# Kernel tuning notes

Hardware: AMD Instinct MI355X
Metric: run time of the kernel (lower is better)

## Reference

```python
import jax, jax.numpy as jnp
import numpy as np

B, N, D, K, H = 4, 128, 256, 128, 32
A, E = 128, 512  # num_atoms, num_edges (edge types)


def _nonlinear(x, W1, b1, W2, b2):
    # torch NonLinear: Linear -> exact GELU -> Linear
    return jax.nn.gelu(x @ W1 + b1, approximate=False) @ W2 + b2


def setup_inputs() -> dict:
    key = jax.random.key(0)
    ks = jax.random.split(key, 32)
    pos = jax.random.normal(ks[0], (B, N, 3), dtype=jnp.float32) * 3.0
    x = jax.random.randint(ks[1], (B, N, 9), 1, A + 1)          # avoid padding idx 0
    node_type_edge = jax.random.randint(ks[2], (B, N, N, 2), 1, E)
    # 9 atom embedding tables, padding_idx=0 rows zeroed
    atom_emb = (jax.random.normal(ks[3], (9, A + 1, D), dtype=jnp.float32) * 0.02).at[:, 0].set(0.0)
    sc = D ** -0.5
    W_la = jax.random.normal(ks[4], (D, D), dtype=jnp.float32) * sc
    W_ra = jax.random.normal(ks[5], (D, D), dtype=jnp.float32) * sc
    W_ld = jax.random.normal(ks[6], (D, D), dtype=jnp.float32) * sc
    W_rd = jax.random.normal(ks[7], (D, D), dtype=jnp.float32) * sc
    gbf_means = jax.random.normal(ks[8], (K,), dtype=jnp.float32)
    gbf_stds = jax.random.uniform(ks[9], (K,), dtype=jnp.float32, minval=0.5, maxval=3.0)
    src_mul = (jax.random.normal(ks[10], (E,), dtype=jnp.float32) * 0.1).at[0].set(0.0)
    tgt_mul = (jax.random.normal(ks[11], (E,), dtype=jnp.float32) * 0.1).at[0].set(0.0)
    src_bias = (jax.random.normal(ks[12], (E,), dtype=jnp.float32) * 0.1).at[0].set(0.0)
    tgt_bias = (jax.random.normal(ks[13], (E,), dtype=jnp.float32) * 0.1).at[0].set(0.0)
    gbf_W1 = jax.random.normal(ks[14], (K, K), dtype=jnp.float32) * (K ** -0.5)
    gbf_b1 = jnp.zeros((K,), jnp.float32)
    gbf_W2 = jax.random.normal(ks[15], (K, H), dtype=jnp.float32) * (K ** -0.5)
    gbf_b2 = jnp.zeros((H,), jnp.float32)
    dih_W1 = jax.random.normal(ks[16], (D, D), dtype=jnp.float32) * sc
    dih_b1 = jnp.zeros((D,), jnp.float32)
    dih_W2 = jax.random.normal(ks[17], (D, H), dtype=jnp.float32) * sc
    dih_b2 = jnp.zeros((H,), jnp.float32)
    ang_W1 = jax.random.normal(ks[18], (D, D), dtype=jnp.float32) * sc
    ang_b1 = jnp.zeros((D,), jnp.float32)
    ang_W2 = jax.random.normal(ks[19], (D, D), dtype=jnp.float32) * sc
    ang_b2 = jnp.zeros((D,), jnp.float32)
    return dict(pos=pos, atom_emb=atom_emb, W_la=W_la, W_ra=W_ra, W_ld=W_ld, W_rd=W_rd,
                gbf_means=gbf_means, gbf_stds=gbf_stds, src_mul=src_mul, tgt_mul=tgt_mul,
                src_bias=src_bias, tgt_bias=tgt_bias, gbf_W1=gbf_W1, gbf_b1=gbf_b1,
                gbf_W2=gbf_W2, gbf_b2=gbf_b2, dih_W1=dih_W1, dih_b1=dih_b1, dih_W2=dih_W2,
                dih_b2=dih_b2, ang_W1=ang_W1, ang_b1=ang_b1, ang_W2=ang_W2, ang_b2=ang_b2,
                x=x, node_type_edge=node_type_edge)


def _forward(pos, atom_emb, W_la, W_ra, W_ld, W_rd, gbf_means, gbf_stds,
             src_mul, tgt_mul, src_bias, tgt_bias, gbf_W1, gbf_b1, gbf_W2, gbf_b2,
             dih_W1, dih_b1, dih_W2, dih_b2, ang_W1, ang_b1, ang_W2, ang_b2,
             x, node_type_edge):
    no_pos = (~jnp.all(pos == 0, axis=(-1, -2))).astype(pos.dtype)  # [B]
    # sum of 9 per-feature embeddings  -> [B, N, D]
    node_feature = sum(atom_emb[i][x[..., i]] for i in range(9))
    padding_mask = jnp.all(x == 0, axis=-1)                         # [B, N]
    # delta_pos[b,i,j] = pos[b,j] - pos[b,i]
    delta_pos = pos[:, None, :, :] - pos[:, :, None, :]             # [B, N, N, 3]
    dist = jnp.linalg.norm(delta_pos, axis=-1)                      # [B, N, N]
    delta_pos = delta_pos / (dist[..., None] + 1e-5)
    # node_vec_feature[b,i,c,d] = node_feature[b,i,d] * sum_j (1-pad_j) delta_pos[b,i,j,c]
    # (exact fusion of edge_vec_feature -> masked sum, since node_feature only depends on i)
    keep = (~padding_mask).astype(pos.dtype)                        # [B, N]
    s = jnp.einsum('bijc,bj->bic', delta_pos, keep)                 # [B, N, 3]
    node_vec = node_feature[:, :, None, :] * s[..., None]           # [B, N, 3, D]
    # angle feature
    angle = jnp.sum((node_vec @ W_la) * (node_vec @ W_ra), axis=-2)  # [B, N, D]
    angle = _nonlinear(angle, ang_W1, ang_b1, ang_W2, ang_b2)
    angle = angle * no_pos[:, None, None]
    # gaussian RPE
    et = node_type_edge
    mul = src_mul[et[..., 0]] + tgt_mul[et[..., 1]]                 # [B, N, N]
    bias = src_bias[et[..., 0]] + tgt_bias[et[..., 1]]
    xg = mul[..., None] * dist[..., None] + bias[..., None]         # [B, N, N, 1] -> K
    std = jnp.abs(gbf_stds) + 0.01
    a = (2.0 * 3.14159) ** 0.5
    edge_feature = jnp.exp(-0.5 * ((xg - gbf_means) / std) ** 2) / (a * std)  # [B,N,N,K]
    gbf_result = _nonlinear(edge_feature, gbf_W1, gbf_b1, gbf_W2, gbf_b2)     # [B,N,N,H]
    # dihedral: vector rejection of projected node vec features onto edge directions
    left = node_vec @ W_ld                                          # [B, N, 3, D]
    right = node_vec @ W_rd
    Ld = jnp.einsum('bjcd,bijc->bijd', left, delta_pos)             # proj of left (indexed j)
    wl = left[:, None] - Ld[..., None, :] * delta_pos[..., None]    # [B, N, N, 3, D]
    Rd = jnp.einsum('bicd,bijc->bijd', right, -delta_pos)           # proj of right (indexed i)
    wr = right[:, :, None] - Rd[..., None, :] * (-delta_pos)[..., None]
    edge_dih = jnp.sum(wl * wr, axis=-2)                            # [B, N, N, D]
    edge_dih = _nonlinear(edge_dih, dih_W1, dih_b1, dih_W2, dih_b2)  # [B, N, N, H]
    attn_bias = (gbf_result + edge_dih) * no_pos[:, None, None, None]
    attn_bias = jnp.transpose(attn_bias, (0, 3, 1, 2))              # [B, H, N, N]
    attn_bias = jnp.where(padding_mask[:, None, None, :], -jnp.inf, attn_bias)
    return attn_bias, angle, delta_pos


def reference(pos, atom_emb, W_la, W_ra, W_ld, W_rd, gbf_means, gbf_stds,
              src_mul, tgt_mul, src_bias, tgt_bias, gbf_W1, gbf_b1, gbf_W2, gbf_b2,
              dih_W1, dih_b1, dih_W2, dih_b2, ang_W1, ang_b1, ang_W2, ang_b2,
              x, node_type_edge):
    return _forward(pos, atom_emb, W_la, W_ra, W_ld, W_rd, gbf_means, gbf_stds,
                    src_mul, tgt_mul, src_bias, tgt_bias, gbf_W1, gbf_b1, gbf_W2, gbf_b2,
                    dih_W1, dih_b1, dih_W2, dih_b2, ang_W1, ang_b1, ang_W2, ang_b2,
                    x, node_type_edge)
```

## Files before the change

kernel.cpp:

```cpp
#include <hip/hip_runtime.h>
#include <math.h>

#define BB 4
#define NN 128
#define DD 256
#define KK 128
#define HH 32
#define AA 128
#define EE 512

typedef float f32x4 __attribute__((ext_vector_type(4)));
typedef short short8 __attribute__((ext_vector_type(8)));

__device__ __forceinline__ float gelu_fast(float x) {
    float x2 = x * x;
    float t = x * fmaf(x2, 0.0713548162726f, 1.59576912161f);
    float e = __expf(-t);
    return x * __builtin_amdgcn_rcpf(1.0f + e);
}

__device__ __forceinline__ unsigned short f2bf(float f) {
    unsigned int u = __float_as_uint(f);
    u = u + 0x7fffu + ((u >> 16) & 1u);
    return (unsigned short)(u >> 16);
}

__device__ __forceinline__ int swz512(int row, int colByte) {
    return row * 512 + (colByte ^ ((row & 7) << 4));
}
__device__ __forceinline__ int swz256(int row, int colByte) {
    return row * 256 + (colByte ^ ((row & 7) << 4));
}

__global__ __launch_bounds__(256) void k_setup(
    const float* __restrict__ pos, const int* __restrict__ x,
    const float* __restrict__ atom_emb,
    const float* __restrict__ dW1, const float* __restrict__ dW2,
    const float* __restrict__ gW1, const float* __restrict__ gW2,
    const float* __restrict__ wla, const float* __restrict__ wra,
    const float* __restrict__ wld, const float* __restrict__ wrd,
    const float* __restrict__ aW1, const float* __restrict__ aW2,
    float* __restrict__ out_dp, float* __restrict__ dist_ws,
    float* __restrict__ s_ws, float* __restrict__ keep, float* __restrict__ no_pos,
    unsigned short* __restrict__ nf_ws, unsigned short* __restrict__ wpack) {
    int blk = blockIdx.x;
    int t = threadIdx.x;

    if (blk < 512) {
        int bi = blk;
        int b = bi >> 7;
        int i = bi & 127;
        __shared__ float red[3][128];
        __shared__ int flag;
        if (t == 0) flag = 0;
        float kj = 0.0f, dx = 0.0f, dy = 0.0f, dz = 0.0f;
        float pjx = 0.0f, pjy = 0.0f, pjz = 0.0f;
        int bj = b * NN + (t & 127);
        if (t < 128) {
            int j = t;
            int allz = 1;
            #pragma unroll
            for (int f = 0; f < 9; ++f) allz &= (x[bj * 9 + f] == 0);
            kj = allz ? 0.0f : 1.0f;
            float pix = pos[bi * 3 + 0], piy = pos[bi * 3 + 1], piz = pos[bi * 3 + 2];
            pjx = pos[bj * 3 + 0]; pjy = pos[bj * 3 + 1]; pjz = pos[bj * 3 + 2];
            dx = pjx - pix; dy = pjy - piy; dz = pjz - piz;
            float dist = sqrtf(dx * dx + dy * dy + dz * dz);
            float inv = 1.0f / (dist + 1e-5f);
            dx *= inv; dy *= inv; dz *= inv;
            size_t e = (size_t)bi * NN + j;
            out_dp[e * 3 + 0] = dx;
            out_dp[e * 3 + 1] = dy;
            out_dp[e * 3 + 2] = dz;
            dist_ws[e] = dist;
            red[0][j] = kj * dx; red[1][j] = kj * dy; red[2][j] = kj * dz;
        }
        __syncthreads();
        if (t < 128) {
            if (pjx != 0.0f || pjy != 0.0f || pjz != 0.0f) flag = 1;
        }
        for (int off = 64; off > 0; off >>= 1) {
            if (t < off) {
                red[0][t] += red[0][t + off];
                red[1][t] += red[1][t + off];
                red[2][t] += red[2][t + off];
            }
            __syncthreads();
        }
        if (t == 0) {
            s_ws[bi * 3 + 0] = red[0][0];
            s_ws[bi * 3 + 1] = red[1][0];
            s_ws[bi * 3 + 2] = red[2][0];
        }
        if (i == 0 && t < 128) {
            keep[bj] = kj;
            if (t == 0) no_pos[b] = flag ? 1.0f : 0.0f;
        }
        return;
    }

    if (blk < 1024) {
        int bn = blk - 512;
        float acc = 0.0f;
        #pragma unroll
        for (int f = 0; f < 9; ++f) {
            int xi = x[bn * 9 + f];
            acc += atom_emb[((size_t)(f * (AA + 1) + xi)) * DD + t];
        }
        nf_ws[(size_t)bn * DD + t] = f2bf(acc);
        return;
    }

    {
        int idx = (blk - 1024) * 256 + t;
        const float* W; int Nc, base, k, c8;
        if (idx < 8192)       { W = dW1; Nc = 256; base = 0;     int li = idx;         k = li >> 5; c8 = li & 31; }
        else if (idx < 9216)  { W = dW2; Nc = 32;  base = 65536; int li = idx - 8192;  k = li >> 2; c8 = li & 3; }
        else if (idx < 11264) { W = gW1; Nc = 128; base = 73728; int li = idx - 9216;  k = li >> 4; c8 = li & 15; }
        else if (idx < 11776) { W = gW2; Nc = 32;  base = 90112; int li = idx - 11264; k = li >> 2; c8 = li & 3; }
        else if (idx < 60928) {
            int q  = (idx - 11776) >> 13;
            int li = (idx - 11776) & 8191;
            W = (q == 0) ? wla : (q == 1) ? wra : (q == 2) ? wld : (q == 3) ? wrd : (q == 4) ? aW1 : aW2;
            Nc = 256; base = 94208 + q * 65536; k = li >> 5; c8 = li & 31;
        }
        else return;
        int ntiles = Nc >> 4;
        int ks = k >> 5, hi = (k & 31) >> 3, ee = k & 7;
        const float* wp = &W[k * Nc + c8 * 8];
        float4 a = *reinterpret_cast<const float4*>(wp);
        float4 b4 = *reinterpret_cast<const float4*>(wp + 4);
        float vals[8] = {a.x, a.y, a.z, a.w, b4.x, b4.y, b4.z, b4.w};
        #pragma unroll
        for (int jj = 0; jj < 8; ++jj) {
            int c = c8 * 8 + jj;
            int nt = c >> 4, lo = c & 15;
            wpack[base + (((ks * ntiles + nt) * 64) + hi * 16 + lo) * 8 + ee] = f2bf(vals[jj]);
        }
    }
}

__device__ __forceinline__ void stage32x256(const unsigned short* __restrict__ src, int bn0,
                                            unsigned short* sA, int t) {
    #pragma unroll
    for (int r = 0; r < 4; ++r) {
        int idx = r * 256 + t;
        int row = idx >> 5;
        int c8 = idx & 31;
        short8 v = *reinterpret_cast<const short8*>(&src[((size_t)(bn0 + row)) * DD + c8 * 8]);
        *reinterpret_cast<short8*>((char*)sA + swz512(row, c8 * 16)) = v;
    }
}

__device__ __forceinline__ void gemm_nt(const unsigned short* __restrict__ Bp, int nt,
                                        const unsigned short* sA, int l, int lo, int hi,
                                        f32x4 acc[2]) {
    for (int ks = 0; ks < 8; ++ks) {
        short8 a0 = *reinterpret_cast<const short8*>((const char*)sA + swz512(lo, ks * 64 + hi * 16));
        short8 a1 = *reinterpret_cast<const short8*>((const char*)sA + swz512(16 + lo, ks * 64 + hi * 16));
        short8 bfr = *reinterpret_cast<const short8*>(&Bp[(((size_t)ks * 16 + nt) * 64 + l) * 8]);
        acc[0] = __builtin_amdgcn_mfma_f32_16x16x32_bf16(a0, bfr, acc[0], 0, 0, 0);
        acc[1] = __builtin_amdgcn_mfma_f32_16x16x32_bf16(a1, bfr, acc[1], 0, 0, 0);
    }
}

__device__ __forceinline__ void gemm_chunk32(const unsigned short* __restrict__ Bp,
                                             const unsigned short* sAp,
                                             int w, int l, int lo, int hi,
                                             f32x4 acc[2][4]) {
    for (int ks = 0; ks < 8; ++ks) {
        short8 a[2];
        #pragma unroll
        for (int m = 0; m < 2; ++m)
            a[m] = *reinterpret_cast<const short8*>((const char*)sAp + swz512(m * 16 + lo, ks * 64 + hi * 16));
        #pragma unroll
        for (int n = 0; n < 4; ++n) {
            short8 bfr = *reinterpret_cast<const short8*>(&Bp[(((size_t)ks * 16 + (w * 4 + n)) * 64 + l) * 8]);
            #pragma unroll
            for (int m = 0; m < 2; ++m)
                acc[m][n] = __builtin_amdgcn_mfma_f32_16x16x32_bf16(a[m], bfr, acc[m][n], 0, 0, 0);
        }
    }
}

__global__ __launch_bounds__(256, 4) void k2a(
    const unsigned short* __restrict__ nf_ws,
    const unsigned short* __restrict__ Wla_p, const unsigned short* __restrict__ Wra_p,
    const unsigned short* __restrict__ Wld_p, const unsigned short* __restrict__ Wrd_p,
    const float* __restrict__ s_ws,
    float* __restrict__ ld_ws, float* __restrict__ rd_ws,
    unsigned short* __restrict__ ap_ws) {
    int blk = blockIdx.x;
    int c = blk & 3, tile = blk >> 2;
    int bn0 = tile * 32;
    int t = threadIdx.x;
    int w = t >> 6, l = t & 63, lo = l & 15, hi = l >> 4;
    int nt = c * 4 + w;

    __shared__ __align__(16) unsigned short sA[32 * 256];
    __shared__ float ls2[32];
    if (t < 32) {
        float a0 = s_ws[(bn0 + t) * 3 + 0];
        float a1 = s_ws[(bn0 + t) * 3 + 1];
        float a2 = s_ws[(bn0 + t) * 3 + 2];
        ls2[t] = a0 * a0 + a1 * a1 + a2 * a2;
    }
    stage32x256(nf_ws, bn0, sA, t);
    __syncthreads();

    f32x4 a_la[2] = {}, a_ra[2] = {}, a_ld[2] = {}, a_rd[2] = {};
    gemm_nt(Wla_p, nt, sA, l, lo, hi, a_la);
    gemm_nt(Wra_p, nt, sA, l, lo, hi, a_ra);
    gemm_nt(Wld_p, nt, sA, l, lo, hi, a_ld);
    gemm_nt(Wrd_p, nt, sA, l, lo, hi, a_rd);

    int col = nt * 16 + lo;
    #pragma unroll
    for (int m = 0; m < 2; ++m) {
        #pragma unroll
        for (int r = 0; r < 4; ++r) {
            int row = m * 16 + hi * 4 + r;
            size_t off = (size_t)(bn0 + row) * DD + col;
            ld_ws[off] = a_ld[m][r];
            rd_ws[off] = a_rd[m][r];
            ap_ws[off] = f2bf(ls2[row] * a_la[m][r] * a_ra[m][r]);
        }
    }
}

__global__ __launch_bounds__(256, 2) void k_mega(
    const unsigned short* __restrict__ Wp1, const unsigned short* __restrict__ Wp2,
    const unsigned short* __restrict__ Wg1, const unsigned short* __restrict__ Wg2,
    const unsigned short* __restrict__ WaW1_p, const unsigned short* __restrict__ WaW2_p,
    const float* __restrict__ dih_b1, const float* __restrict__ dih_b2,
    const float* __restrict__ gbf_b1, const float* __restrict__ gbf_b2,
    const float* __restrict__ ang_b1, const float* __restrict__ ang_b2,
    const float* __restrict__ gbf_means, const float* __restrict__ gbf_stds,
    const float* __restrict__ src_mul, const float* __restrict__ tgt_mul,
    const float* __restrict__ src_bias, const float* __restrict__ tgt_bias,
    const int* __restrict__ nte,
    const unsigned short* __restrict__ ap_ws,
    const float* __restrict__ ld_ws, const float* __restrict__ rd_ws,
    const float* __restrict__ s_ws, const float* __restrict__ dist_ws,
    const float* __restrict__ keep, const float* __restrict__ no_pos,
    const float* __restrict__ dp_in,
    float* __restrict__ out_angle, float* __restrict__ out_attn) {
    int t = threadIdx.x;
    int w  = t >> 6;
    int l  = t & 63;
    int lo = l & 15;
    int hi = l >> 4;

    __shared__ __align__(16) unsigned short sE[64 * 256];
    __shared__ __align__(16) unsigned short sH[64 * 256];
    __shared__ __align__(16) float rd_l[DD];
    __shared__ float sg[64], sxg[64], skeep[64];
    __shared__ __align__(16) float lmean[KK], linv[KK], lcoef[KK];

    if (blockIdx.x < 16) {
        int tile = blockIdx.x;
        int bn0 = tile * 32;
        stage32x256(ap_ws, bn0, sE, t);
        __syncthreads();
        {
            f32x4 acc[2][4] = {};
            gemm_chunk32(WaW1_p, sE, w, l, lo, hi, acc);
            #pragma unroll
            for (int n = 0; n < 4; ++n) {
                int col = w * 64 + n * 16 + lo;
                float b1v = ang_b1[col];
                #pragma unroll
                for (int m = 0; m < 2; ++m)
                    #pragma unroll
                    for (int r = 0; r < 4; ++r) {
                        int row = m * 16 + hi * 4 + r;
                        *reinterpret_cast<unsigned short*>((char*)sH + swz512(row, col * 2)) =
                            f2bf(gelu_fast(acc[m][n][r] + b1v));
                    }
            }
        }
        __syncthreads();
        {
            f32x4 acc[2][4] = {};
            gemm_chunk32(WaW2_p, sH, w, l, lo, hi, acc);
            float lnp = no_pos[tile >> 2];
            #pragma unroll
            for (int n = 0; n < 4; ++n) {
                int col = w * 64 + n * 16 + lo;
                float b2v = ang_b2[col];
                #pragma unroll
                for (int m = 0; m < 2; ++m)
                    #pragma unroll
                    for (int r = 0; r < 4; ++r) {
                        int row = m * 16 + hi * 4 + r;
                        out_angle[(size_t)(bn0 + row) * DD + col] = (acc[m][n][r] + b2v) * lnp;
                    }
            }
        }
        return;
    }

    int blk = blockIdx.x - 16;
    int jh = blk & 1;
    int i  = (blk >> 1) & 127;
    int b  = blk >> 8;
    int j0 = jh * 64;

    int bi = b * NN + i;

    if (t < 64) {
        int j = j0 + t;
        size_t e = (size_t)bi * NN + j;
        float d0 = dp_in[e * 3 + 0], d1 = dp_in[e * 3 + 1], d2 = dp_in[e * 3 + 2];
        float si0 = s_ws[bi * 3 + 0], si1 = s_ws[bi * 3 + 1], si2 = s_ws[bi * 3 + 2];
        int bj = b * NN + j;
        float sj0 = s_ws[bj * 3 + 0], sj1 = s_ws[bj * 3 + 1], sj2 = s_ws[bj * 3 + 2];
        float u = sj0 * d0 + sj1 * d1 + sj2 * d2;
        float v = si0 * d0 + si1 * d1 + si2 * d2;
        float dp2 = d0 * d0 + d1 * d1 + d2 * d2;
        sg[t] = (si0 * sj0 + si1 * sj1 + si2 * sj2) - u * v * (2.0f - dp2);
        int et0 = nte[e * 2 + 0], et1 = nte[e * 2 + 1];
        sxg[t] = (src_mul[et0] + tgt_mul[et1]) * dist_ws[e] + src_bias[et0] + tgt_bias[et1];
        skeep[t] = keep[bj];
    } else if (t < 128) {
        int q = t - 64;
        reinterpret_cast<float4*>(rd_l)[q] =
            reinterpret_cast<const float4*>(&rd_ws[(size_t)bi * DD])[q];
    } else {
        int k = t - 128;
        float s = fabsf(gbf_stds[k]) + 0.01f;
        lmean[k] = gbf_means[k];
        linv[k] = 1.0f / s;
        lcoef[k] = 1.0f / (2.5066262f * s);
    }
    __syncthreads();

    {
        const float* ldbase = &ld_ws[((size_t)(b * NN + j0)) * DD];
        #pragma unroll
        for (int r = 0; r < 8; ++r) {
            int idx = r * 256 + t;
            int row = idx >> 5;
            int c8  = idx & 31;
            float g = sg[row];
            const float* lp = ldbase + row * DD + c8 * 8;
            float4 l0 = *reinterpret_cast<const float4*>(lp);
            float4 l1 = *reinterpret_cast<const float4*>(lp + 4);
            float4 r0 = *reinterpret_cast<const float4*>(&rd_l[c8 * 8]);
            float4 r1 = *reinterpret_cast<const float4*>(&rd_l[c8 * 8 + 4]);
            short8 vv;
            vv[0] = (short)f2bf(g * l0.x * r0.x);
            vv[1] = (short)f2bf(g * l0.y * r0.y);
            vv[2] = (short)f2bf(g * l0.z * r0.z);
            vv[3] = (short)f2bf(g * l0.w * r0.w);
            vv[4] = (short)f2bf(g * l1.x * r1.x);
            vv[5] = (short)f2bf(g * l1.y * r1.y);
            vv[6] = (short)f2bf(g * l1.z * r1.z);
            vv[7] = (short)f2bf(g * l1.w * r1.w);
            *reinterpret_cast<short8*>((char*)sE + swz512(row, c8 * 16)) = vv;
        }
        unsigned short* sG = sH;
        #pragma unroll
        for (int r = 0; r < 4; ++r) {
            int idx = r * 256 + t;
            int row = idx >> 4;
            int c8  = idx & 15;
            float xv = sxg[row];
            float4 m0 = *reinterpret_cast<const float4*>(&lmean[c8 * 8]);
            float4 m1 = *reinterpret_cast<const float4*>(&lmean[c8 * 8 + 4]);
            float4 i0 = *reinterpret_cast<const float4*>(&linv[c8 * 8]);
            float4 i1 = *reinterpret_cast<const float4*>(&linv[c8 * 8 + 4]);
            float4 c0 = *reinterpret_cast<const float4*>(&lcoef[c8 * 8]);
            float4 c1 = *reinterpret_cast<const float4*>(&lcoef[c8 * 8 + 4]);
            float z;
            short8 vv;
            z = (xv - m0.x) * i0.x; vv[0] = (short)f2bf(c0.x * __expf(-0.5f * z * z));
            z = (xv - m0.y) * i0.y; vv[1] = (short)f2bf(c0.y * __expf(-0.5f * z * z));
            z = (xv - m0.z) * i0.z; vv[2] = (short)f2bf(c0.z * __expf(-0.5f * z * z));
            z = (xv - m0.w) * i0.w; vv[3] = (short)f2bf(c0.w * __expf(-0.5f * z * z));
            z = (xv - m1.x) * i1.x; vv[4] = (short)f2bf(c1.x * __expf(-0.5f * z * z));
            z = (xv - m1.y) * i1.y; vv[5] = (short)f2bf(c1.y * __expf(-0.5f * z * z));
            z = (xv - m1.z) * i1.z; vv[6] = (short)f2bf(c1.z * __expf(-0.5f * z * z));
            z = (xv - m1.w) * i1.w; vv[7] = (short)f2bf(c1.w * __expf(-0.5f * z * z));
            *reinterpret_cast<short8*>((char*)sG + swz256(row, c8 * 16)) = vv;
        }
    }
    __syncthreads();

    f32x4 accg[4][2] = {};
    {
        const unsigned short* sG = sH;
        for (int ks = 0; ks < 4; ++ks) {
            short8 a[4];
            #pragma unroll
            for (int m = 0; m < 4; ++m)
                a[m] = *reinterpret_cast<const short8*>((const char*)sG + swz256(m * 16 + lo, ks * 64 + hi * 16));
            #pragma unroll
            for (int n = 0; n < 2; ++n) {
                short8 bfr = *reinterpret_cast<const short8*>(&Wg1[(((size_t)ks * 8 + (w * 2 + n)) * 64 + l) * 8]);
                #pragma unroll
                for (int m = 0; m < 4; ++m)
                    accg[m][n] = __builtin_amdgcn_mfma_f32_16x16x32_bf16(a[m], bfr, accg[m][n], 0, 0, 0);
            }
        }
    }
    f32x4 acc[4][4] = {};
    for (int ks = 0; ks < 8; ++ks) {
        short8 a[4];
        #pragma unroll
        for (int m = 0; m < 4; ++m)
            a[m] = *reinterpret_cast<const short8*>((const char*)sE + swz512(m * 16 + lo, ks * 64 + hi * 16));
        #pragma unroll
        for (int n = 0; n < 4; ++n) {
            short8 bfr = *reinterpret_cast<const short8*>(&Wp1[(((size_t)ks * 16 + (w * 4 + n)) * 64 + l) * 8]);
            #pragma unroll
            for (int m = 0; m < 4; ++m)
                acc[m][n] = __builtin_amdgcn_mfma_f32_16x16x32_bf16(a[m], bfr, acc[m][n], 0, 0, 0);
        }
    }
    __syncthreads();

    {
        #pragma unroll
        for (int n = 0; n < 4; ++n) {
            int col = w * 64 + n * 16 + lo;
            float b1v = dih_b1[col];
            #pragma unroll
            for (int m = 0; m < 4; ++m) {
                int row0 = m * 16 + hi * 4;
                #pragma unroll
                for (int r = 0; r < 4; ++r) {
                    *reinterpret_cast<unsigned short*>((char*)sH + swz512(row0 + r, col * 2)) =
                        f2bf(gelu_fast(acc[m][n][r] + b1v));
                }
            }
        }
        unsigned short* sGH = sE;
        #pragma unroll
        for (int n = 0; n < 2; ++n) {
            int col = w * 32 + n * 16 + lo;
            float b1v = gbf_b1[col];
            #pragma unroll
            for (int m = 0; m < 4; ++m) {
                int row0 = m * 16 + hi * 4;
                #pragma unroll
                for (int r = 0; r < 4; ++r) {
                    *reinterpret_cast<unsigned short*>((char*)sGH + swz256(row0 + r, col * 2)) =
                        f2bf(gelu_fast(accg[m][n][r] + b1v));
                }
            }
        }
    }
    __syncthreads();

    f32x4 acc2d[2] = {};
    for (int ks = 0; ks < 8; ++ks) {
        short8 a = *reinterpret_cast<const short8*>((const char*)sH + swz512(w * 16 + lo, ks * 64 + hi * 16));
        #pragma unroll
        for (int n = 0; n < 2; ++n) {
            short8 bfr = *reinterpret_cast<const short8*>(&Wp2[(((size_t)ks * 2 + n) * 64 + l) * 8]);
            acc2d[n] = __builtin_amdgcn_mfma_f32_16x16x32_bf16(a, bfr, acc2d[n], 0, 0, 0);
        }
    }
    f32x4 acc2g[2] = {};
    {
        const unsigned short* sGH = sE;
        for (int ks = 0; ks < 4; ++ks) {
            short8 a = *reinterpret_cast<const short8*>((const char*)sGH + swz256(w * 16 + lo, ks * 64 + hi * 16));
            #pragma unroll
            for (int n = 0; n < 2; ++n) {
                short8 bfr = *reinterpret_cast<const short8*>(&Wg2[(((size_t)ks * 2 + n) * 64 + l) * 8]);
                acc2g[n] = __builtin_amdgcn_mfma_f32_16x16x32_bf16(a, bfr, acc2g[n], 0, 0, 0);
            }
        }
    }

    float npos = no_pos[b];
    int e0 = w * 16 + hi * 4;
    #pragma unroll
    for (int n = 0; n < 2; ++n) {
        int h = n * 16 + lo;
        float bsum = dih_b2[h] + gbf_b2[h];
        float4 v;
        float vr;
        vr = (acc2d[n][0] + acc2g[n][0] + bsum) * npos; v.x = (skeep[e0 + 0] == 0.0f) ? -INFINITY : vr;
        vr = (acc2d[n][1] + acc2g[n][1] + bsum) * npos; v.y = (skeep[e0 + 1] == 0.0f) ? -INFINITY : vr;
        vr = (acc2d[n][2] + acc2g[n][2] + bsum) * npos; v.z = (skeep[e0 + 2] == 0.0f) ? -INFINITY : vr;
        vr = (acc2d[n][3] + acc2g[n][3] + bsum) * npos; v.w = (skeep[e0 + 3] == 0.0f) ? -INFINITY : vr;
        *reinterpret_cast<float4*>(&out_attn[(((size_t)b * HH + h) * NN + i) * NN + j0 + e0]) = v;
    }
}

extern "C" void kernel_launch(void* const* d_in, const int* in_sizes, int n_in,
                              void* d_out, int out_size, void* d_ws, size_t ws_size,
                              hipStream_t stream) {
    const float* pos       = (const float*)d_in[0];
    const float* atom_emb  = (const float*)d_in[1];
    const float* W_la      = (const float*)d_in[2];
    const float* W_ra      = (const float*)d_in[3];
    const float* W_ld      = (const float*)d_in[4];
    const float* W_rd      = (const float*)d_in[5];
    const float* gbf_means = (const float*)d_in[6];
    const float* gbf_stds  = (const float*)d_in[7];
    const float* src_mul   = (const float*)d_in[8];
    const float* tgt_mul   = (const float*)d_in[9];
    const float* src_bias  = (const float*)d_in[10];
    const float* tgt_bias  = (const float*)d_in[11];
    const float* gbf_W1    = (const float*)d_in[12];
    const float* gbf_b1    = (const float*)d_in[13];
    const float* gbf_W2    = (const float*)d_in[14];
    const float* gbf_b2    = (const float*)d_in[15];
    const float* dih_W1    = (const float*)d_in[16];
    const float* dih_b1    = (const float*)d_in[17];
    const float* dih_W2    = (const float*)d_in[18];
    const float* dih_b2    = (const float*)d_in[19];
    const float* ang_W1    = (const float*)d_in[20];
    const float* ang_b1    = (const float*)d_in[21];
    const float* ang_W2    = (const float*)d_in[22];
    const float* ang_b2    = (const float*)d_in[23];
    const int*   x         = (const int*)d_in[24];
    const int*   nte       = (const int*)d_in[25];

    float* out = (float*)d_out;
    float* out_attn  = out;
    float* out_angle = out + (size_t)BB * HH * NN * NN;
    float* out_dp    = out_angle + (size_t)BB * NN * DD;

    float* ws = (float*)d_ws;
    float* keep    = ws;
    float* no_pos  = ws + 512;
    float* s_ws    = ws + 1024;
    float* dist_ws = ws + 4096;
    float* ld_ws   = ws + 4096 + 65536;
    float* rd_ws   = ld_ws + (size_t)BB * NN * DD;
    unsigned short* wp = (unsigned short*)(ws + 331776);
    unsigned short* Wp1    = wp;
    unsigned short* Wp2    = wp + 65536;
    unsigned short* Wg1    = wp + 73728;
    unsigned short* Wg2    = wp + 90112;
    unsigned short* Wla_p  = wp + 94208;
    unsigned short* Wra_p  = wp + 159744;
    unsigned short* Wld_p  = wp + 225280;
    unsigned short* Wrd_p  = wp + 290816;
    unsigned short* WaW1_p = wp + 356352;
    unsigned short* WaW2_p = wp + 421888;
    unsigned short* nf_ws  = (unsigned short*)(ws + 575488);
    unsigned short* ap_ws  = (unsigned short*)(ws + 641024);

    k_setup<<<dim3(1262), dim3(256), 0, stream>>>(
        pos, x, atom_emb, dih_W1, dih_W2, gbf_W1, gbf_W2,
        W_la, W_ra, W_ld, W_rd, ang_W1, ang_W2,
        out_dp, dist_ws, s_ws, keep, no_pos, nf_ws, wp);
    k2a<<<dim3(64), dim3(256), 0, stream>>>(nf_ws, Wla_p, Wra_p, Wld_p, Wrd_p,
                                            s_ws, ld_ws, rd_ws, ap_ws);
    k_mega<<<dim3(16 + BB * NN * 2), dim3(256), 0, stream>>>(
        Wp1, Wp2, Wg1, Wg2, WaW1_p, WaW2_p,
        dih_b1, dih_b2, gbf_b1, gbf_b2, ang_b1, ang_b2,
        gbf_means, gbf_stds, src_mul, tgt_mul, src_bias, tgt_bias, nte,
        ap_ws, ld_ws, rd_ws, s_ws, dist_ws, keep, no_pos, out_dp,
        out_angle, out_attn);
}
```

Baseline: 149.5 us.

## Halve k_mega hidden LDS buffer to raise occupancy and split k2a work per wave

Result: no change. 148.3 us (-0.8%).

```diff
diff --git a/kernel.cpp b/kernel.cpp
--- a/kernel.cpp
+++ b/kernel.cpp
@@ -191,13 +191,14 @@
     float* __restrict__ ld_ws, float* __restrict__ rd_ws,
     unsigned short* __restrict__ ap_ws) {
     int blk = blockIdx.x;
-    int c = blk & 3, tile = blk >> 2;
+    int nt = blk & 15, tile = blk >> 4;
     int bn0 = tile * 32;
     int t = threadIdx.x;
     int w = t >> 6, l = t & 63, lo = l & 15, hi = l >> 4;
-    int nt = c * 4 + w;
 
     __shared__ __align__(16) unsigned short sA[32 * 256];
+    __shared__ float sLA[32][16];
+    __shared__ float sRA[32][16];
     __shared__ float ls2[32];
     if (t < 32) {
         float a0 = s_ws[(bn0 + t) * 3 + 0];
@@ -208,27 +209,39 @@
     stage32x256(nf_ws, bn0, sA, t);
     __syncthreads();
 
-    f32x4 a_la[2] = {}, a_ra[2] = {}, a_ld[2] = {}, a_rd[2] = {};
-    gemm_nt(Wla_p, nt, sA, l, lo, hi, a_la);
-    gemm_nt(Wra_p, nt, sA, l, lo, hi, a_ra);
-    gemm_nt(Wld_p, nt, sA, l, lo, hi, a_ld);
-    gemm_nt(Wrd_p, nt, sA, l, lo, hi, a_rd);
+    const unsigned short* Bp = (w == 0) ? Wla_p : (w == 1) ? Wra_p : (w == 2) ? Wld_p : Wrd_p;
+    f32x4 acc[2] = {};
+    gemm_nt(Bp, nt, sA, l, lo, hi, acc);
 
     int col = nt * 16 + lo;
-    #pragma unroll
-    for (int m = 0; m < 2; ++m) {
-        #pragma unroll
-        for (int r = 0; r < 4; ++r) {
-            int row = m * 16 + hi * 4 + r;
-            size_t off = (size_t)(bn0 + row) * DD + col;
-            ld_ws[off] = a_ld[m][r];
-            rd_ws[off] = a_rd[m][r];
-            ap_ws[off] = f2bf(ls2[row] * a_la[m][r] * a_ra[m][r]);
-        }
-    }
-}
-
-__global__ __launch_bounds__(256, 2) void k_mega(
+    if (w == 0 || w == 1) {
+        float (*dst)[16] = (w == 0) ? sLA : sRA;
+        #pragma unroll
+        for (int m = 0; m < 2; ++m)
+            #pragma unroll
+            for (int r = 0; r < 4; ++r)
+                dst[m * 16 + hi * 4 + r][lo] = acc[m][r];
+    } else {
+        float* dstg = (w == 2) ? ld_ws : rd_ws;
+        #pragma unroll
+        for (int m = 0; m < 2; ++m)
+            #pragma unroll
+            for (int r = 0; r < 4; ++r)
+                dstg[(size_t)(bn0 + m * 16 + hi * 4 + r) * DD + col] = acc[m][r];
+    }
+    __syncthreads();
+
+    if (w == 0) {
+        #pragma unroll
+        for (int r8 = 0; r8 < 8; ++r8) {
+            int row = hi * 8 + r8;
+            ap_ws[(size_t)(bn0 + row) * DD + nt * 16 + lo] =
+                f2bf(ls2[row] * sLA[row][lo] * sRA[row][lo]);
+        }
+    }
+}
+
+__global__ __launch_bounds__(256, 3) void k_mega(
     const unsigned short* __restrict__ Wp1, const unsigned short* __restrict__ Wp2,
     const unsigned short* __restrict__ Wg1, const unsigned short* __restrict__ Wg2,
     const unsigned short* __restrict__ WaW1_p, const unsigned short* __restrict__ WaW2_p,
@@ -252,7 +265,7 @@
     int hi = l >> 4;
 
     __shared__ __align__(16) unsigned short sE[64 * 256];
-    __shared__ __align__(16) unsigned short sH[64 * 256];
+    __shared__ __align__(16) unsigned short sH2[64 * 128];
     __shared__ __align__(16) float rd_l[DD];
     __shared__ float sg[64], sxg[64], skeep[64];
     __shared__ __align__(16) float lmean[KK], linv[KK], lcoef[KK];
@@ -274,7 +287,7 @@
                     #pragma unroll
                     for (int r = 0; r < 4; ++r) {
                         int row = m * 16 + hi * 4 + r;
-                        *reinterpret_cast<unsigned short*>((char*)sH + swz512(row, col * 2)) =
+                        *reinterpret_cast<unsigned short*>((char*)sH2 + swz512(row, col * 2)) =
                             f2bf(gelu_fast(acc[m][n][r] + b1v));
                     }
             }
@@ -282,7 +295,7 @@
         __syncthreads();
         {
             f32x4 acc[2][4] = {};
-            gemm_chunk32(WaW2_p, sH, w, l, lo, hi, acc);
+            gemm_chunk32(WaW2_p, sH2, w, l, lo, hi, acc);
             float lnp = no_pos[tile >> 2];
             #pragma unroll
             for (int n = 0; n < 4; ++n) {
@@ -359,7 +372,6 @@
             vv[7] = (short)f2bf(g * l1.w * r1.w);
             *reinterpret_cast<short8*>((char*)sE + swz512(row, c8 * 16)) = vv;
         }
-        unsigned short* sG = sH;
         #pragma unroll
         for (int r = 0; r < 4; ++r) {
             int idx = r * 256 + t;
@@ -382,26 +394,23 @@
             z = (xv - m1.y) * i1.y; vv[5] = (short)f2bf(c1.y * __expf(-0.5f * z * z));
             z = (xv - m1.z) * i1.z; vv[6] = (short)f2bf(c1.z * __expf(-0.5f * z * z));
             z = (xv - m1.w) * i1.w; vv[7] = (short)f2bf(c1.w * __expf(-0.5f * z * z));
-            *reinterpret_cast<short8*>((char*)sG + swz256(row, c8 * 16)) = vv;
+            *reinterpret_cast<short8*>((char*)sH2 + swz256(row, c8 * 16)) = vv;
         }
     }
     __syncthreads();
 
     f32x4 accg[4][2] = {};
-    {
-        const unsigned short* sG = sH;
-        for (int ks = 0; ks < 4; ++ks) {
-            short8 a[4];
+    for (int ks = 0; ks < 4; ++ks) {
+        short8 a[4];
+        #pragma unroll
+        for (int m = 0; m < 4; ++m)
+            a[m] = *reinterpret_cast<const short8*>((const char*)sH2 + swz256(m * 16 + lo, ks * 64 + hi * 16));
+        #pragma unroll
+        for (int n = 0; n < 2; ++n) {
+            short8 bfr = *reinterpret_cast<const short8*>(&Wg1[(((size_t)ks * 8 + (w * 2 + n)) * 64 + l) * 8]);
             #pragma unroll
             for (int m = 0; m < 4; ++m)
-                a[m] = *reinterpret_cast<const short8*>((const char*)sG + swz256(m * 16 + lo, ks * 64 + hi * 16));
-            #pragma unroll
-            for (int n = 0; n < 2; ++n) {
-                short8 bfr = *reinterpret_cast<const short8*>(&Wg1[(((size_t)ks * 8 + (w * 2 + n)) * 64 + l) * 8]);
-                #pragma unroll
-                for (int m = 0; m < 4; ++m)
-                    accg[m][n] = __builtin_amdgcn_mfma_f32_16x16x32_bf16(a[m], bfr, accg[m][n], 0, 0, 0);
-            }
+                accg[m][n] = __builtin_amdgcn_mfma_f32_16x16x32_bf16(a[m], bfr, accg[m][n], 0, 0, 0);
         }
     }
     f32x4 acc[4][4] = {};
@@ -421,20 +430,6 @@
     __syncthreads();
 
     {
-        #pragma unroll
-        for (int n = 0; n < 4; ++n) {
-            int col = w * 64 + n * 16 + lo;
-            float b1v = dih_b1[col];
-            #pragma unroll
-            for (int m = 0; m < 4; ++m) {
-                int row0 = m * 16 + hi * 4;
-                #pragma unroll
-                for (int r = 0; r < 4; ++r) {
-                    *reinterpret_cast<unsigned short*>((char*)sH + swz512(row0 + r, col * 2)) =
-                        f2bf(gelu_fast(acc[m][n][r] + b1v));
-                }
-            }
-        }
         unsigned short* sGH = sE;
         #pragma unroll
         for (int n = 0; n < 2; ++n) {
@@ -450,18 +445,25 @@
                 }
             }
         }
-    }
-    __syncthreads();
-
-    f32x4 acc2d[2] = {};
-    for (int ks = 0; ks < 8; ++ks) {
-        short8 a = *reinterpret_cast<const short8*>((const char*)sH + swz512(w * 16 + lo, ks * 64 + hi * 16));
-        #pragma unroll
-        for (int n = 0; n < 2; ++n) {
-            short8 bfr = *reinterpret_cast<const short8*>(&Wp2[(((size_t)ks * 2 + n) * 64 + l) * 8]);
-            acc2d[n] = __builtin_amdgcn_mfma_f32_16x16x32_bf16(a, bfr, acc2d[n], 0, 0, 0);
-        }
-    }
+        if (w < 2) {
+            #pragma unroll
+            for (int n = 0; n < 4; ++n) {
+                int col = w * 64 + n * 16 + lo;
+                float b1v = dih_b1[col];
+                #pragma unroll
+                for (int m = 0; m < 4; ++m) {
+                    int row0 = m * 16 + hi * 4;
+                    #pragma unroll
+                    for (int r = 0; r < 4; ++r) {
+                        *reinterpret_cast<unsigned short*>((char*)sH2 + swz256(row0 + r, col * 2)) =
+                            f2bf(gelu_fast(acc[m][n][r] + b1v));
+                    }
+                }
+            }
+        }
+    }
+    __syncthreads();
+
     f32x4 acc2g[2] = {};
     {
         const unsigned short* sGH = sE;
@@ -472,6 +474,44 @@
                 short8 bfr = *reinterpret_cast<const short8*>(&Wg2[(((size_t)ks * 2 + n) * 64 + l) * 8]);
                 acc2g[n] = __builtin_amdgcn_mfma_f32_16x16x32_bf16(a, bfr, acc2g[n], 0, 0, 0);
             }
+        }
+    }
+    f32x4 acc2d[2] = {};
+    for (int ks = 0; ks < 4; ++ks) {
+        short8 a = *reinterpret_cast<const short8*>((const char*)sH2 + swz256(w * 16 + lo, ks * 64 + hi * 16));
+        #pragma unroll
+        for (int n = 0; n < 2; ++n) {
+            short8 bfr = *reinterpret_cast<const short8*>(&Wp2[(((size_t)ks * 2 + n) * 64 + l) * 8]);
+            acc2d[n] = __builtin_amdgcn_mfma_f32_16x16x32_bf16(a, bfr, acc2d[n], 0, 0, 0);
+        }
+    }
+    __syncthreads();
+
+    if (w >= 2) {
+        #pragma unroll
+        for (int n = 0; n < 4; ++n) {
+            int col = w * 64 + n * 16 + lo;
+            float b1v = dih_b1[col];
+            int hcol = col - 128;
+            #pragma unroll
+            for (int m = 0; m < 4; ++m) {
+                int row0 = m * 16 + hi * 4;
+                #pragma unroll
+                for (int r = 0; r < 4; ++r) {
+                    *reinterpret_cast<unsigned short*>((char*)sH2 + swz256(row0 + r, hcol * 2)) =
+                        f2bf(gelu_fast(acc[m][n][r] + b1v));
+                }
+            }
+        }
+    }
+    __syncthreads();
+
+    for (int ks = 0; ks < 4; ++ks) {
+        short8 a = *reinterpret_cast<const short8*>((const char*)sH2 + swz256(w * 16 + lo, ks * 64 + hi * 16));
+        #pragma unroll
+        for (int n = 0; n < 2; ++n) {
+            short8 bfr = *reinterpret_cast<const short8*>(&Wp2[(((size_t)(ks + 4) * 2 + n) * 64 + l) * 8]);
+            acc2d[n] = __builtin_amdgcn_mfma_f32_16x16x32_bf16(a, bfr, acc2d[n], 0, 0, 0);
         }
     }
 
@@ -551,8 +591,8 @@
         pos, x, atom_emb, dih_W1, dih_W2, gbf_W1, gbf_W2,
         W_la, W_ra, W_ld, W_rd, ang_W1, ang_W2,
         out_dp, dist_ws, s_ws, keep, no_pos, nf_ws, wp);
-    k2a<<<dim3(64), dim3(256), 0, stream>>>(nf_ws, Wla_p, Wra_p, Wld_p, Wrd_p,
-                                            s_ws, ld_ws, rd_ws, ap_ws);
+    k2a<<<dim3(256), dim3(256), 0, stream>>>(nf_ws, Wla_p, Wra_p, Wld_p, Wrd_p,
+                                             s_ws, ld_ws, rd_ws, ap_ws);
     k_mega<<<dim3(16 + BB * NN * 2), dim3(256), 0, stream>>>(
         Wp1, Wp2, Wg1, Wg2, WaW1_p, WaW2_p,
         dih_b1, dih_b2, gbf_b1, gbf_b2, ang_b1, ang_b2,
```
